# Kernel optimization log

Hardware: AMD Instinct MI355X
Metric: run time of the kernel (lower is better)

The kernel has to match this reference:

```python
import jax, jax.numpy as jnp
import numpy as np

N = 100_000      # nodes
E = 1_600_000    # edges (avg degree 16)
DIN = 128
DOUT = 128
NEG_SLOPE = 0.2  # DGL GATConv default negative_slope


def setup_inputs() -> dict:
    key = jax.random.key(0)
    k1, k2, k3, k4, k5, k6 = jax.random.split(key, 6)
    h = jax.random.normal(k1, (N, DIN), dtype=jnp.float32)
    src = jax.random.randint(k2, (E,), 0, N, dtype=jnp.int32)
    dst = jax.random.randint(k3, (E,), 0, N, dtype=jnp.int32)
    W = jax.random.normal(k4, (DIN, DOUT), dtype=jnp.float32) / np.sqrt(DIN).astype(np.float32)
    attn_l = jax.random.normal(k5, (DOUT,), dtype=jnp.float32) * 0.1
    attn_r = jax.random.normal(k6, (DOUT,), dtype=jnp.float32) * 0.1
    return {"h": h, "src": src, "dst": dst, "W": W, "attn_l": attn_l, "attn_r": attn_r}


def reference(h, src, dst, W, attn_l, attn_r):
    # Single-head DGL GATConv (bias=False, no feat/attn dropout, no activation).
    feat = h @ W                                   # [N, D] projected features
    el = feat @ attn_l                             # [N] source attention logits
    er = feat @ attn_r                             # [N] destination attention logits
    e = jax.nn.leaky_relu(el[src] + er[dst], NEG_SLOPE)   # [E] edge scores

    # Numerically stable edge softmax, grouped by destination node.
    m = jax.ops.segment_max(e, dst, num_segments=N)        # [N]
    m = jnp.where(jnp.isfinite(m), m, 0.0)                 # nodes with no in-edges
    ex = jnp.exp(e - m[dst])                               # [E]
    denom = jax.ops.segment_sum(ex, dst, num_segments=N)   # [N]
    alpha = ex / jnp.maximum(denom[dst], jnp.float32(1e-9))  # [E]

    # Weighted aggregation of source features into destination nodes.
    out = jax.ops.segment_sum(alpha[:, None] * feat[src], dst, num_segments=N)  # [N, D]
    return out
```

## Files before the change

### kernel.cpp

```cpp
#include <hip/hip_runtime.h>
#include <hip/hip_bf16.h>

#define N_NODES 100000
#define N_EDGES 1600000
#define D 128
#define NEG_SLOPE 0.2f

#define NBKT 1563
#define CAPB 2048
#define BCHUNK 4096
#define BIN_BLOCKS 391
#define GEMM_BLOCKS 782
#define CAP 1536

typedef __attribute__((ext_vector_type(8))) short s8v;
typedef __attribute__((ext_vector_type(4))) float f4v;

static __device__ __forceinline__ unsigned short f2bf(float f) {
    __hip_bfloat16 b = __float2bfloat16(f);
    return *(unsigned short*)&b;
}
static __device__ __forceinline__ float bflo(unsigned int u) {
    return __uint_as_float(u << 16);
}
static __device__ __forceinline__ float bfhi(unsigned int u) {
    return __uint_as_float(u & 0xffff0000u);
}

__global__ __launch_bounds__(256) void wcast(
    const float* __restrict__ W, const float* __restrict__ attn_l,
    const float* __restrict__ attn_r, unsigned short* __restrict__ Wt)
{
    const int t = threadIdx.x;
    if (blockIdx.x < 16) {
        const int n0 = blockIdx.x * 8;
#pragma unroll
        for (int i = 0; i < 4; ++i) {
            const int id = t + 256 * i;
            const int n = n0 + (id >> 7), k = id & 127;
            Wt[n * 128 + k] = f2bf(W[k * 128 + n]);
        }
    } else {
        __shared__ float all[128], arl[128];
        if (t < 128) { all[t] = attn_l[t]; arl[t] = attn_r[t]; }
        __syncthreads();
        if (t < 128) {
            float sl = 0.f, sr = 0.f;
            for (int n = 0; n < 128; ++n) {
                const float v = W[t * 128 + n];
                sl += v * all[n]; sr += v * arl[n];
            }
            Wt[128 * 128 + t] = f2bf(sl);
            Wt[129 * 128 + t] = f2bf(sr);
        }
    }
}

__global__ __launch_bounds__(512) void gemm_bin(
    const float* __restrict__ h, const unsigned short* __restrict__ Wt,
    unsigned short* __restrict__ featb, float* __restrict__ el, float* __restrict__ er,
    const int* __restrict__ src, const int* __restrict__ dst,
    int* __restrict__ gwp, unsigned int* __restrict__ eb)
{
    __shared__ __align__(16) char smem[69632];
    const int t = threadIdx.x;

    if (blockIdx.x < BIN_BLOCKS) {
        int* cnt_l            = (int*)smem;
        int* lbase            = (int*)(smem + 6256);
        int* gbase            = (int*)(smem + 12528);
        int* tmp              = (int*)(smem + 18784);
        unsigned int* slocal  = (unsigned int*)(smem + 26976);
        unsigned short* sbkt  = (unsigned short*)(smem + 43360);

        const int base = (int)blockIdx.x * BCHUNK;
        const int nloc = min(BCHUNK, N_EDGES - base);

        for (int i = t; i < NBKT; i += 512) cnt_l[i] = 0;
        __syncthreads();

        unsigned int ent[8];
        unsigned short bk[8];
#pragma unroll
        for (int j = 0; j < 8; ++j) {
            const int i = t + 512 * j;
            if (i < nloc) {
                const int s = src[base + i];
                const int d = dst[base + i];
                bk[j]  = (unsigned short)(d >> 6);
                ent[j] = (unsigned int)s | ((unsigned int)(d & 63) << 17);
                atomicAdd(&cnt_l[bk[j]], 1);
            } else bk[j] = 0xffff;
        }
        __syncthreads();

#pragma unroll
        for (int j = 0; j < 4; ++j) {
            const int i = t + 512 * j;
            tmp[i] = (i < NBKT) ? cnt_l[i] : 0;
        }
        __syncthreads();
        for (int o = 1; o < 2048; o <<= 1) {
            int a[4];
#pragma unroll
            for (int j = 0; j < 4; ++j) {
                const int i = t + 512 * j;
                a[j] = (i >= o) ? tmp[i - o] : 0;
            }
            __syncthreads();
#pragma unroll
            for (int j = 0; j < 4; ++j) tmp[t + 512 * j] += a[j];
            __syncthreads();
        }
        for (int i = t; i < NBKT; i += 512) lbase[i] = (i == 0) ? 0 : tmp[i - 1];
        if (t == 0) lbase[NBKT] = tmp[NBKT - 1];
        __syncthreads();

        for (int b = t; b < NBKT; b += 512) {
            const int c = lbase[b + 1] - lbase[b];
            if (c) gbase[b] = b * CAPB + atomicAdd(&gwp[b], c);
            cnt_l[b] = 0;
        }
        __syncthreads();

#pragma unroll
        for (int j = 0; j < 8; ++j) {
            if (bk[j] != 0xffff) {
                const int p = lbase[bk[j]] + atomicAdd(&cnt_l[bk[j]], 1);
                slocal[p] = ent[j];
                sbkt[p]   = bk[j];
            }
        }
        __syncthreads();

        for (int i = t; i < nloc; i += 512) {
            const int b = sbkt[i];
            eb[gbase[b] + (i - lbase[b])] = slocal[i];
        }
    } else {
        unsigned short* Asmem = (unsigned short*)smem;
        unsigned short* Bsmem = (unsigned short*)(smem + 32768);

        const int w    = t >> 6;
        const int lane = t & 63;
        const int g4   = lane >> 4;
        const int cl   = lane & 15;
        const int row0 = ((int)blockIdx.x - BIN_BLOCKS) * 128;

#pragma unroll
        for (int i = 0; i < 4; ++i) {
            const int ch = t + 512 * i;
            const int r = ch >> 4, c = ch & 15;
            const int srow = min(row0 + r, N_NODES - 1);
            const float4 a = *(const float4*)&h[srow * D + c * 8];
            const float4 b = *(const float4*)&h[srow * D + c * 8 + 4];
            s8v v;
            v[0] = (short)f2bf(a.x); v[1] = (short)f2bf(a.y);
            v[2] = (short)f2bf(a.z); v[3] = (short)f2bf(a.w);
            v[4] = (short)f2bf(b.x); v[5] = (short)f2bf(b.y);
            v[6] = (short)f2bf(b.z); v[7] = (short)f2bf(b.w);
            *(s8v*)&Asmem[r * 128 + ((c ^ (r & 15)) << 3)] = v;
        }
        for (int ch = t; ch < 2080; ch += 512) {
            const int n = ch >> 4, c = ch & 15;
            *(s8v*)&Bsmem[n * 128 + ((c ^ (n & 15)) << 3)] =
                *(const s8v*)&Wt[n * 128 + c * 8];
        }
        __syncthreads();

        f4v acc[9] = {};
#pragma unroll
        for (int ks = 0; ks < 4; ++ks) {
            const int c = ks * 4 + g4;
            s8v bfr[9];
#pragma unroll
            for (int nt = 0; nt < 9; ++nt) {
                const int n = nt * 16 + cl;
                bfr[nt] = *(const s8v*)&Bsmem[n * 128 + ((c ^ cl) << 3)];
            }
            const int r = w * 16 + cl;
            const s8v af = *(const s8v*)&Asmem[r * 128 + ((c ^ cl) << 3)];
#pragma unroll
            for (int nt = 0; nt < 9; ++nt)
                acc[nt] = __builtin_amdgcn_mfma_f32_16x16x32_bf16(
                    af, bfr[nt], acc[nt], 0, 0, 0);
        }

        unsigned short* ftile = Asmem;
#pragma unroll
        for (int nt = 0; nt < 8; ++nt) {
            const int ch = 2 * nt + (cl >> 3);
#pragma unroll
            for (int reg = 0; reg < 4; ++reg) {
                const int r = w * 16 + 4 * g4 + reg;
                ftile[r * 128 + ((ch ^ (r & 15)) << 3) + (cl & 7)] =
                    f2bf(acc[nt][reg]);
            }
        }
        if (cl < 2) {
            float* dstp = (cl == 0) ? el : er;
#pragma unroll
            for (int reg = 0; reg < 4; ++reg) {
                const int rg = row0 + w * 16 + 4 * g4 + reg;
                if (rg < N_NODES) dstp[rg] = acc[8][reg];
            }
        }
        __syncthreads();
#pragma unroll
        for (int i = 0; i < 4; ++i) {
            const int ch = t + 512 * i;
            const int r = ch >> 4, c = ch & 15;
            if (row0 + r < N_NODES)
                *(s8v*)&featb[(row0 + r) * 128 + c * 8] =
                    *(const s8v*)&ftile[r * 128 + ((c ^ (r & 15)) << 3)];
        }
    }
}

__global__ __launch_bounds__(512) void aggregate(
    const int* __restrict__ gwp, const unsigned int* __restrict__ eb,
    const float* __restrict__ el, const float* __restrict__ er,
    const uint2* __restrict__ featb2, float* __restrict__ out)
{
    __shared__ __align__(8) uint2 sw[CAP];
    __shared__ int off_l[65];
    __shared__ int cnt_l[64];
    __shared__ float nsum[64];
    __shared__ float er_l[64];

    const int t = threadIdx.x;
    const int b = blockIdx.x;
    const int ne   = gwp[b];
    const int gbeg = b * CAPB;
    const int node0 = b << 6;
    const int w    = t >> 6;
    const int lane = t & 63;
    const int ll   = lane & 31;
    const int half = lane >> 5;

    if (t < 64) {
        const int nd = node0 + t;
        er_l[t] = (nd < N_NODES) ? er[nd] : 0.f;
        cnt_l[t] = 0;
        nsum[t] = 0.f;
    }
    __syncthreads();

    if (ne <= CAP) {
        unsigned int ent[3];
#pragma unroll
        for (int j = 0; j < 3; ++j) {
            const int i = t + 512 * j;
            if (i < ne) {
                ent[j] = eb[gbeg + i];
                atomicAdd(&cnt_l[(ent[j] >> 17) & 63], 1);
            }
        }
        __syncthreads();
        if (w == 0) {
            const int v = cnt_l[lane];
            int inc = v;
#pragma unroll
            for (int o = 1; o < 64; o <<= 1) {
                const int u = __shfl_up(inc, o, 64);
                if (lane >= o) inc += u;
            }
            off_l[lane] = inc - v;
            if (lane == 63) off_l[64] = inc;
            cnt_l[lane] = 0;
        }
        __syncthreads();
#pragma unroll
        for (int j = 0; j < 3; ++j) {
            const int i = t + 512 * j;
            if (i < ne) {
                const unsigned int e = ent[j];
                const int dl = (e >> 17) & 63;
                const int sj = (int)(e & 0x1FFFFu);
                float sc = el[sj] + er_l[dl];
                sc = (sc > 0.f) ? sc : NEG_SLOPE * sc;
                const float ex = __expf(sc);
                const int p = off_l[dl] + atomicAdd(&cnt_l[dl], 1);
                sw[p] = make_uint2(e, __float_as_uint(ex));
                atomicAdd(&nsum[dl], ex);
            }
        }
        __syncthreads();

        for (int dl = w; dl < 64; dl += 8) {
            const int node = node0 + dl;
            if (node >= N_NODES) break;
            const int beg = off_l[dl];
            const int n   = off_l[dl + 1] - beg;
            float4 acc = make_float4(0.f, 0.f, 0.f, 0.f);
            const int iters = (n + 1) >> 1;
            for (int tt = 0; tt < iters; ++tt) {
                const int idx = 2 * tt + half;
                const uint2 p = sw[beg + min(idx, n - 1)];
                const float wj = (idx < n) ? __uint_as_float(p.y) : 0.f;
                const int  sjj = (int)(p.x & 0x1FFFFu);
                const uint2 fb = featb2[sjj * 32 + ll];
                acc.x += wj * bflo(fb.x); acc.y += wj * bfhi(fb.x);
                acc.z += wj * bflo(fb.y); acc.w += wj * bfhi(fb.y);
            }
            acc.x += __shfl_xor(acc.x, 32, 64);
            acc.y += __shfl_xor(acc.y, 32, 64);
            acc.z += __shfl_xor(acc.z, 32, 64);
            acc.w += __shfl_xor(acc.w, 32, 64);
            const float rs = 1.f / fmaxf(nsum[dl], 1e-9f);
            if (lane < 32)
                *(float4*)&out[node * D + ll * 4] =
                    make_float4(acc.x * rs, acc.y * rs, acc.z * rs, acc.w * rs);
        }
    } else {
        for (int dl = w; dl < 64; dl += 8) {
            const int node = node0 + dl;
            if (node >= N_NODES) break;
            float4 acc = make_float4(0.f, 0.f, 0.f, 0.f);
            float ssum = 0.f;
            for (int ch = 0; ch < ne; ch += 64) {
                const int nn = min(64, ne - ch);
                float ex = 0.f; int sj = 0;
                if (lane < nn) {
                    const unsigned int e = eb[gbeg + ch + lane];
                    if ((int)((e >> 17) & 63) == dl) {
                        sj = (int)(e & 0x1FFFFu);
                        float sc = el[sj] + er_l[dl];
                        sc = (sc > 0.f) ? sc : NEG_SLOPE * sc;
                        ex = __expf(sc);
                    }
                }
                ssum += ex;
                const int iters = (nn + 1) >> 1;
                for (int tt = 0; tt < iters; ++tt) {
                    const int idx = 2 * tt + half;
                    const float wj = __shfl(ex, idx, 64);
                    const int  sjj = __shfl(sj, idx, 64);
                    if (wj > 0.f) {
                        const uint2 fb = featb2[sjj * 32 + ll];
                        acc.x += wj * bflo(fb.x); acc.y += wj * bfhi(fb.x);
                        acc.z += wj * bflo(fb.y); acc.w += wj * bfhi(fb.y);
                    }
                }
            }
#pragma unroll
            for (int o = 1; o < 64; o <<= 1) ssum += __shfl_xor(ssum, o, 64);
            acc.x += __shfl_xor(acc.x, 32, 64);
            acc.y += __shfl_xor(acc.y, 32, 64);
            acc.z += __shfl_xor(acc.z, 32, 64);
            acc.w += __shfl_xor(acc.w, 32, 64);
            const float rs = 1.f / fmaxf(ssum, 1e-9f);
            if (lane < 32)
                *(float4*)&out[node * D + ll * 4] =
                    make_float4(acc.x * rs, acc.y * rs, acc.z * rs, acc.w * rs);
        }
    }
}

extern "C" void kernel_launch(void* const* d_in, const int* in_sizes, int n_in,
                              void* d_out, int out_size, void* d_ws, size_t ws_size,
                              hipStream_t stream)
{
    const float* h      = (const float*)d_in[0];
    const int*   src    = (const int*)  d_in[1];
    const int*   dst    = (const int*)  d_in[2];
    const float* W      = (const float*)d_in[3];
    const float* attn_l = (const float*)d_in[4];
    const float* attn_r = (const float*)d_in[5];
    float* out = (float*)d_out;

    char* ws = (char*)d_ws;
    unsigned short* featb = (unsigned short*)ws; ws += (size_t)N_NODES * D * 2;
    unsigned short* Wt    = (unsigned short*)ws; ws += (size_t)130 * 128 * 2;
    ws = (char*)(((size_t)ws + 15) & ~(size_t)15);
    float* el  = (float*)ws; ws += (size_t)N_NODES * sizeof(float);
    float* er  = (float*)ws; ws += (size_t)N_NODES * sizeof(float);
    int*   gwp = (int*)ws;   ws += (size_t)NBKT * sizeof(int);
    ws = (char*)(((size_t)ws + 15) & ~(size_t)15);
    unsigned int* eb = (unsigned int*)ws; ws += (size_t)NBKT * CAPB * sizeof(unsigned int);

    hipMemsetAsync(gwp, 0, (size_t)NBKT * sizeof(int), stream);

    wcast<<<17, 256, 0, stream>>>(W, attn_l, attn_r, Wt);
    gemm_bin<<<BIN_BLOCKS + GEMM_BLOCKS, 512, 0, stream>>>(
        h, Wt, featb, el, er, src, dst, gwp, eb);
    aggregate<<<NBKT, 512, 0, stream>>>(gwp, eb, el, er, (const uint2*)featb, out);
}
```

Before: 210.9 us.

## Fold counter zeroing into wcast, double bin chunk, use wave-shuffle scan

Removes the separate hipMemsetAsync by zeroing the per-bucket write counters in two extra wcast blocks, saving one stream operation. Doubles the edges each binning block handles (8192 instead of 4096), halving the bin block count and the per-block global atomics on bucket counters. Replaces the 11-step shared-memory Hillis-Steele scan over bucket counts with a per-thread 4-element sum, a wave shuffle scan and a cross-wave fixup, cutting barriers. The costs are more registers per thread (16 entries), fewer bin blocks to spread across CUs, and a larger shared-memory footprint.

New measurement: 196.9 us. 1.07x faster.

```diff
diff --git a/kernel.cpp b/kernel.cpp
--- a/kernel.cpp
+++ b/kernel.cpp
@@ -8,8 +8,8 @@
 
 #define NBKT 1563
 #define CAPB 2048
-#define BCHUNK 4096
-#define BIN_BLOCKS 391
+#define BCHUNK 8192
+#define BIN_BLOCKS 196
 #define GEMM_BLOCKS 782
 #define CAP 1536
 
@@ -29,7 +29,8 @@
 
 __global__ __launch_bounds__(256) void wcast(
     const float* __restrict__ W, const float* __restrict__ attn_l,
-    const float* __restrict__ attn_r, unsigned short* __restrict__ Wt)
+    const float* __restrict__ attn_r, unsigned short* __restrict__ Wt,
+    int* __restrict__ gwp)
 {
     const int t = threadIdx.x;
     if (blockIdx.x < 16) {
@@ -40,7 +41,7 @@
             const int n = n0 + (id >> 7), k = id & 127;
             Wt[n * 128 + k] = f2bf(W[k * 128 + n]);
         }
-    } else {
+    } else if (blockIdx.x == 16) {
         __shared__ float all[128], arl[128];
         if (t < 128) { all[t] = attn_l[t]; arl[t] = attn_r[t]; }
         __syncthreads();
@@ -52,6 +53,12 @@
             }
             Wt[128 * 128 + t] = f2bf(sl);
             Wt[129 * 128 + t] = f2bf(sr);
+        }
+    } else {
+        const int base = (int)(blockIdx.x - 17) * 800;
+        for (int i = t; i < 800; i += 256) {
+            const int b = base + i;
+            if (b < NBKT) gwp[b] = 0;
         }
     }
 }
@@ -68,21 +75,23 @@
     if (blockIdx.x < BIN_BLOCKS) {
         int* cnt_l            = (int*)smem;
         int* lbase            = (int*)(smem + 6256);
-        int* gbase            = (int*)(smem + 12528);
-        int* tmp              = (int*)(smem + 18784);
-        unsigned int* slocal  = (unsigned int*)(smem + 26976);
-        unsigned short* sbkt  = (unsigned short*)(smem + 43360);
-
+        int* gbase            = (int*)(smem + 12512);
+        int* wsum             = (int*)(smem + 18768);
+        unsigned int* slocal  = (unsigned int*)(smem + 18832);
+        unsigned short* sbkt  = (unsigned short*)(smem + 51600);
+
+        const int w    = t >> 6;
+        const int lane = t & 63;
         const int base = (int)blockIdx.x * BCHUNK;
         const int nloc = min(BCHUNK, N_EDGES - base);
 
         for (int i = t; i < NBKT; i += 512) cnt_l[i] = 0;
         __syncthreads();
 
-        unsigned int ent[8];
-        unsigned short bk[8];
-#pragma unroll
-        for (int j = 0; j < 8; ++j) {
+        unsigned int ent[16];
+        unsigned short bk[16];
+#pragma unroll
+        for (int j = 0; j < 16; ++j) {
             const int i = t + 512 * j;
             if (i < nloc) {
                 const int s = src[base + i];
@@ -94,26 +103,33 @@
         }
         __syncthreads();
 
-#pragma unroll
-        for (int j = 0; j < 4; ++j) {
-            const int i = t + 512 * j;
-            tmp[i] = (i < NBKT) ? cnt_l[i] : 0;
-        }
-        __syncthreads();
-        for (int o = 1; o < 2048; o <<= 1) {
-            int a[4];
-#pragma unroll
-            for (int j = 0; j < 4; ++j) {
-                const int i = t + 512 * j;
-                a[j] = (i >= o) ? tmp[i - o] : 0;
-            }
+        {
+            const int i0 = 4 * t;
+            const int s0 = (i0 + 0 < NBKT) ? cnt_l[i0 + 0] : 0;
+            const int s1 = (i0 + 1 < NBKT) ? cnt_l[i0 + 1] : 0;
+            const int s2 = (i0 + 2 < NBKT) ? cnt_l[i0 + 2] : 0;
+            const int s3 = (i0 + 3 < NBKT) ? cnt_l[i0 + 3] : 0;
+            const int lsum = s0 + s1 + s2 + s3;
+            int inc = lsum;
+#pragma unroll
+            for (int o = 1; o < 64; o <<= 1) {
+                const int u = __shfl_up(inc, o, 64);
+                if (lane >= o) inc += u;
+            }
+            if (lane == 63) wsum[w] = inc;
             __syncthreads();
-#pragma unroll
-            for (int j = 0; j < 4; ++j) tmp[t + 512 * j] += a[j];
+            if (t == 0) {
+                int run = 0;
+#pragma unroll
+                for (int k = 0; k < 8; ++k) { const int v = wsum[k]; wsum[k] = run; run += v; }
+            }
             __syncthreads();
-        }
-        for (int i = t; i < NBKT; i += 512) lbase[i] = (i == 0) ? 0 : tmp[i - 1];
-        if (t == 0) lbase[NBKT] = tmp[NBKT - 1];
+            int b0 = wsum[w] + (inc - lsum);
+            if (i0 + 0 <= NBKT) lbase[i0 + 0] = b0;
+            if (i0 + 1 <= NBKT) lbase[i0 + 1] = b0 + s0;
+            if (i0 + 2 <= NBKT) lbase[i0 + 2] = b0 + s0 + s1;
+            if (i0 + 3 <= NBKT) lbase[i0 + 3] = b0 + s0 + s1 + s2;
+        }
         __syncthreads();
 
         for (int b = t; b < NBKT; b += 512) {
@@ -124,7 +140,7 @@
         __syncthreads();
 
 #pragma unroll
-        for (int j = 0; j < 8; ++j) {
+        for (int j = 0; j < 16; ++j) {
             if (bk[j] != 0xffff) {
                 const int p = lbase[bk[j]] + atomicAdd(&cnt_l[bk[j]], 1);
                 slocal[p] = ent[j];
@@ -379,9 +395,7 @@
     ws = (char*)(((size_t)ws + 15) & ~(size_t)15);
     unsigned int* eb = (unsigned int*)ws; ws += (size_t)NBKT * CAPB * sizeof(unsigned int);
 
-    hipMemsetAsync(gwp, 0, (size_t)NBKT * sizeof(int), stream);
-
-    wcast<<<17, 256, 0, stream>>>(W, attn_l, attn_r, Wt);
+    wcast<<<19, 256, 0, stream>>>(W, attn_l, attn_r, Wt, gwp);
     gemm_bin<<<BIN_BLOCKS + GEMM_BLOCKS, 512, 0, stream>>>(
         h, Wt, featb, el, er, src, dst, gwp, eb);
     aggregate<<<NBKT, 512, 0, stream>>>(gwp, eb, el, er, (const uint2*)featb, out);
```
